# Performance work log

Hardware: AMD Instinct MI355X
Metric: run time of the kernel (lower is better)

Reference implementation:

```python
import jax, jax.numpy as jnp
import numpy as np

N_QUBITS = 6
N_LAYERS = 2
QSVT_DEGREE = 3
BATCH = 128
SEQ_LEN = 512
DIM = 2 ** N_QUBITS
# wire 0 is the most-significant bit in the statevector index (PennyLane convention)
_POP = np.array([bin(i).count('1') for i in range(DIM)], dtype=np.float32)
PHASE_SIGN = jnp.asarray(N_QUBITS - 2.0 * _POP)  # (DIM,): sum_w (1 - 2*bit_w)


def _rx(t):
    c = jnp.cos(0.5 * t).astype(jnp.complex64)
    s = (-1j * jnp.sin(0.5 * t)).astype(jnp.complex64)
    return jnp.stack([jnp.stack([c, s]), jnp.stack([s, c])])


def _ry(t):
    c = jnp.cos(0.5 * t).astype(jnp.complex64)
    s = jnp.sin(0.5 * t).astype(jnp.complex64)
    return jnp.stack([jnp.stack([c, -s]), jnp.stack([s, c])])


def _rz(t):
    e = jnp.exp(-0.5j * t.astype(jnp.complex64))
    z = jnp.zeros((), jnp.complex64)
    return jnp.stack([jnp.stack([e, z]), jnp.stack([z, jnp.conj(e)])])


def _apply_1q(psi, U, w):
    # psi: (B,) + (2,)*N_QUBITS ; U: (2,2) complex, same for all batch elems
    psi = jnp.moveaxis(psi, 1 + w, -1)
    psi = psi @ U.T
    return jnp.moveaxis(psi, -1, 1 + w)


def _apply_ry_batched(psi, theta, w):
    # RY with a per-batch angle theta: (B,)
    psi = jnp.moveaxis(psi, 1 + w, -1)
    c = jnp.cos(0.5 * theta).reshape((-1,) + (1,) * (N_QUBITS - 1))
    s = jnp.sin(0.5 * theta).reshape((-1,) + (1,) * (N_QUBITS - 1))
    a, b = psi[..., 0], psi[..., 1]
    psi = jnp.stack([c * a - s * b, s * a + c * b], axis=-1)
    return jnp.moveaxis(psi, -1, 1 + w)


def _cnot(psi, c, t):
    p0 = jax.lax.index_in_dim(psi, 0, axis=1 + c, keepdims=True)
    p1 = jax.lax.index_in_dim(psi, 1, axis=1 + c, keepdims=True)
    p1 = jnp.flip(p1, axis=1 + t)
    return jnp.concatenate([p0, p1], axis=1 + c)


def _circuit_step(h, x, params, poly):
    # h, x: (B, N_QUBITS) angles. Returns <Z_w> per qubit: (B, N_QUBITS).
    B = h.shape[0]
    # 1) state encoding: RY(h_w)|0> = cos(h/2)|0> + sin(h/2)|1>  (product state)
    c, s = jnp.cos(0.5 * h), jnp.sin(0.5 * h)
    psi = jnp.ones((B, 1), jnp.complex64)
    for w in range(N_QUBITS):
        amp = jnp.stack([c[:, w], s[:, w]], axis=-1).astype(jnp.complex64)  # (B,2)
        psi = (psi[:, :, None] * amp[:, None, :]).reshape(B, -1)
    psi = psi.reshape((B,) + (2,) * N_QUBITS)
    # 2) QSVT block: RZ(coeff*pi) on every wire fuses into one diagonal phase
    for d in range(QSVT_DEGREE + 1):
        theta = poly[d] * np.pi
        phase = jnp.exp((-0.5j) * theta * PHASE_SIGN)  # (DIM,)
        psi = (psi.reshape(B, -1) * phase[None, :]).reshape((B,) + (2,) * N_QUBITS)
        for i in range(N_QUBITS - 1):
            psi = _cnot(psi, i, i + 1)
        psi = _cnot(psi, N_QUBITS - 1, 0)  # ring closure
    # 3) variational layers: per-wire RZ@RY@RX (RX applied first), then CNOT chain
    idx = 0
    for _ in range(N_LAYERS):
        for i in range(N_QUBITS):
            U = _rz(params[idx + 2]) @ _ry(params[idx + 1]) @ _rx(params[idx])
            psi = _apply_1q(psi, U, i)
            idx += 3
        for i in range(N_QUBITS - 1):
            psi = _cnot(psi, i, i + 1)
    # 4) input injection: RY(x_w) with per-batch angles
    for w in range(N_QUBITS):
        psi = _apply_ry_batched(psi, x[:, w], w)
    # 5) measurement: <Z_w> = P(bit_w=0) - P(bit_w=1)
    p = jnp.abs(psi) ** 2
    zs = []
    for w in range(N_QUBITS):
        axes = tuple(a for a in range(1, N_QUBITS + 1) if a != 1 + w)
        pw = p.sum(axis=axes)  # (B,2)
        zs.append(pw[:, 0] - pw[:, 1])
    return jnp.stack(zs, axis=-1)


def _ssm_pass(angles, params, poly, reverse):
    a = jnp.flip(angles, axis=1) if reverse else angles
    xs = jnp.moveaxis(a, 1, 0)  # (T, B, n)
    h0 = jnp.zeros((a.shape[0], N_QUBITS), jnp.float32)

    def step(h, x):
        hn = _circuit_step(h, x, params, poly)
        return hn, hn

    _, ys = jax.lax.scan(step, h0, xs)
    out = jnp.moveaxis(ys, 0, 1)  # (B, T, n)
    return jnp.flip(out, axis=1) if reverse else out


def setup_inputs() -> dict:
    key = jax.random.key(0)
    k0, k1, k2, k3 = jax.random.split(key, 4)
    angles = jax.random.uniform(k0, (BATCH, SEQ_LEN, N_QUBITS), jnp.float32) * np.float32(np.pi)
    poly_coeffs = jax.random.normal(k1, (QSVT_DEGREE + 1,), jnp.float32) * 0.1
    fwd_params = jax.random.normal(k2, (N_QUBITS * N_LAYERS * 3,), jnp.float32) * 0.1
    bwd_params = jax.random.normal(k3, (N_QUBITS * N_LAYERS * 3,), jnp.float32) * 0.1
    fwd_coeff = jnp.full((1,), 0.5, jnp.float32)
    bwd_coeff = jnp.full((1,), 0.5, jnp.float32)
    return {'angles': angles, 'poly_coeffs': poly_coeffs, 'fwd_params': fwd_params,
            'bwd_params': bwd_params, 'fwd_coeff': fwd_coeff, 'bwd_coeff': bwd_coeff}


def reference(angles, poly_coeffs, fwd_params, bwd_params, fwd_coeff, bwd_coeff):
    h_fwd = _ssm_pass(angles, fwd_params, poly_coeffs, reverse=False)
    h_bwd = _ssm_pass(angles, bwd_params, poly_coeffs, reverse=True)
    return jax.nn.sigmoid(fwd_coeff) * h_fwd + jax.nn.sigmoid(bwd_coeff) * h_bwd
```

## Files before the change

kernel.cpp:

```cpp
#include <hip/hip_runtime.h>
#include <hip/hip_bf16.h>
#include <stdint.h>

#define BATCH 128
#define SEQ   512
#define NW    6
#define DIM   64
#define NELEM (BATCH * SEQ * NW)
#define PI_F  3.14159265358979323846f

template <int CTRL>
__device__ __forceinline__ void red_stage6(float v[6]) {
#pragma unroll
    for (int w = 0; w < 6; ++w)
        v[w] += __int_as_float(__builtin_amdgcn_update_dpp(
            0, __float_as_int(v[w]), CTRL, 0xF, 0xF, false));
}

__device__ __forceinline__ void sincos_half(float h, float& s, float& c) {
    const float u = h * h;
    c = fmaf(u, fmaf(u, fmaf(u, -2.1701389e-5f, 2.6041667e-3f), -0.125f), 1.0f);
    s = h * fmaf(u, fmaf(u, fmaf(u, -1.5501e-6f, 2.6041667e-4f), -2.0833333e-2f), 0.5f);
}

__global__ void k_detect(const uint32_t* __restrict__ a, int* __restrict__ flag) {
    __shared__ int cnt;
    if (threadIdx.x == 0) cnt = 0;
    __syncthreads();
    uint32_t w = a[threadIdx.x];
    uint32_t e = (w >> 8) & 0xFFu;
    if (e >= 0x3Au && e <= 0x41u) atomicAdd(&cnt, 1);
    __syncthreads();
    if (threadIdx.x == 0) *flag = (cnt >= 128) ? 1 : 0;
}

__device__ __forceinline__ float ldf(const void* p, int i, bool bf) {
    if (bf) {
        uint32_t u = (uint32_t)((const uint16_t*)p)[i];
        return __uint_as_float(u << 16);
    }
    return ((const float*)p)[i];
}

__global__ void k_convert(const void* ang, const void* poly, const void* fp,
                          const void* bp, const void* fc, const void* bc,
                          float* __restrict__ cs, float* __restrict__ misc,
                          const int* __restrict__ flag) {
    const bool bf = (*flag != 0);
    const int i = blockIdx.x * blockDim.x + threadIdx.x;
    if (i < NELEM) {
        float x = ldf(ang, i, bf);
        float s, c;
        __sincosf(x, &s, &c);
        cs[2 * i]     = c;
        cs[2 * i + 1] = s;
    }
    if (i < 4)                    misc[i]            = ldf(poly, i, bf);
    else if (i >= 64 && i < 100)  misc[4 + (i - 64)] = ldf(fp, i - 64, bf);
    else if (i >= 128 && i < 164) misc[40 + (i - 128)] = ldf(bp, i - 128, bf);
    else if (i == 200)            misc[76] = ldf(fc, 0, bf);
    else if (i == 201)            misc[77] = ldf(bc, 0, bf);
}

__global__ void __launch_bounds__(64) k_msetup(const float* __restrict__ misc,
                                               float* __restrict__ Mg) {
    const int p   = threadIdx.x;
    const int col = blockIdx.x & 63;
    const int dir = blockIdx.x >> 6;
    const float* poly = misc;
    const float* prm  = misc + (dir ? 40 : 4);

    float yr = (p == col) ? 1.f : 0.f;
    float yi = 0.f;

#pragma unroll
    for (int d = 0; d < 4; ++d) {
        const float th = 0.5f * PI_F * poly[d] *
                         (float)(6 - 2 * (int)__popc((unsigned)p));
        float s, c;
        __sincosf(th, &s, &c);
        const float nr = yr * c + yi * s;
        const float ni = yi * c - yr * s;
        yr = nr; yi = ni;
#pragma unroll
        for (int k = 0; k < 6; ++k) {
            const int cw = k, tw = (k + 1) % 6;
            const int src = p ^ (((p >> (5 - cw)) & 1) << (5 - tw));
            yr = __shfl(yr, src, 64);
            yi = __shfl(yi, src, 64);
        }
    }

    int idx = 0;
#pragma unroll
    for (int l = 0; l < 2; ++l) {
#pragma unroll
        for (int w = 0; w < 6; ++w) {
            float cx, sx, cy, sy, cz, sz;
            __sincosf(0.5f * prm[idx + 0], &sx, &cx);
            __sincosf(0.5f * prm[idx + 1], &sy, &cy);
            __sincosf(0.5f * prm[idx + 2], &sz, &cz);
            idx += 3;
            const float A = cy * cx, B = sy * sx, C = sy * cx, D = cy * sx;
            const float U00r = cz * A + sz * B, U00i = cz * B - sz * A;
            const float U11r = U00r,            U11i = sz * A - cz * B;
            const float Xr   = cz * C + sz * D, Xi   = sz * C - cz * D;
            const int m  = 1 << (5 - w);
            const int bb = (p >> (5 - w)) & 1;
            const float C1r = bb ? U11r : U00r;
            const float C1i = bb ? U11i : U00i;
            const float C2r = bb ? Xr : -Xr;
            const float C2i = Xi;
            const float pr = __shfl_xor(yr, m, 64);
            const float pi = __shfl_xor(yi, m, 64);
            const float nr = C1r * yr - C1i * yi + C2r * pr - C2i * pi;
            const float ni = C1r * yi + C1i * yr + C2r * pi + C2i * pr;
            yr = nr; yi = ni;
        }
#pragma unroll
        for (int k = 0; k < 5; ++k) {
            const int src = p ^ (((p >> (5 - k)) & 1) << (5 - (k + 1)));
            yr = __shfl(yr, src, 64);
            yi = __shfl(yi, src, 64);
        }
    }

    float* out = Mg + ((size_t)(dir * 64 + p) * 64 + (size_t)col) * 2;
    out[0] = yr;
    out[1] = yi;
}

__global__ void __launch_bounds__(256, 1) k_sim(const float* __restrict__ cs,
                                                const float* __restrict__ Mg,
                                                float* __restrict__ hbuf) {
    const int tid   = threadIdx.x;
    const int lane  = tid & 63;
    const int wv    = tid >> 6;
    const int chain = blockIdx.x;
    const int dir   = chain >> 7;
    const int b     = chain & 127;
    float* orow = hbuf + (size_t)dir * NELEM + (size_t)b * (SEQ * NW);
    const float* csrow = cs + (size_t)b * (SEQ * NW * 2);

    __shared__ float  cl[SEQ * 12];
    __shared__ float  zb[SEQ * 6];
    __shared__ float  xs[DIM];
    __shared__ float2 pY[4][DIM];

    {
        const float4* src = (const float4*)csrow;
        float4* dst = (float4*)cl;
#pragma unroll
        for (int k = 0; k < 6; ++k) {
            const int idx = tid + k * 256;
            dst[idx] = src[idx];
        }
    }

    float2 Mc[16];
    {
        const float2* mrow =
            (const float2*)(Mg + ((size_t)(dir * 64 + lane) * 64 + wv * 16) * 2);
#pragma unroll
        for (int k = 0; k < 16; ++k) Mc[k] = mrow[k];
    }
    __syncthreads();

    int zmask[6];
#pragma unroll
    for (int w = 0; w < 6; ++w) zmask[w] = ((lane >> (5 - w)) & 1) << 31;
    bool EB[6];
#pragma unroll
    for (int w = 0; w < 6; ++w) EB[w] = (lane >> (5 - w)) & 1;

    float h[6] = {0.f, 0.f, 0.f, 0.f, 0.f, 0.f};

    for (int t = 0; t < SEQ; ++t) {
        if (wv == 0) {
            float amp = 1.f;
#pragma unroll
            for (int w = 0; w < 6; ++w) {
                float s, c;
                sincos_half(h[w], s, c);
                amp *= EB[w] ? s : c;
            }
            xs[lane] = amp;
        }
        __syncthreads();

        {
            const float4* xc = (const float4*)(xs + wv * 16);
            const float4 x0 = xc[0], x1 = xc[1], x2 = xc[2], x3 = xc[3];
            float xv[16];
            xv[0] = x0.x; xv[1] = x0.y; xv[2]  = x0.z; xv[3]  = x0.w;
            xv[4] = x1.x; xv[5] = x1.y; xv[6]  = x1.z; xv[7]  = x1.w;
            xv[8] = x2.x; xv[9] = x2.y; xv[10] = x2.z; xv[11] = x2.w;
            xv[12] = x3.x; xv[13] = x3.y; xv[14] = x3.z; xv[15] = x3.w;
            float2 acc = {0.f, 0.f};
#pragma unroll
            for (int j = 0; j < 16; ++j) {
                acc.x = fmaf(xv[j], Mc[j].x, acc.x);
                acc.y = fmaf(xv[j], Mc[j].y, acc.y);
            }
            pY[wv][lane] = acc;
        }
        __syncthreads();

        if (wv == 0) {
            const int tin = dir ? (SEQ - 1 - t) : t;

            const float4* xr4 = (const float4*)(cl + tin * 12);
            const float4 xq0 = xr4[0], xq1 = xr4[1], xq2 = xr4[2];

            const float2 y0 = pY[0][lane], y1 = pY[1][lane];
            const float2 y2 = pY[2][lane], y3 = pY[3][lane];
            const float yr = (y0.x + y1.x) + (y2.x + y3.x);
            const float yi = (y0.y + y1.y) + (y2.y + y3.y);

            float pr[6], pi[6];
#pragma unroll
            for (int w = 0; w < 6; ++w) pr[w] = __shfl_xor(yr, 1 << (5 - w), 64);
#pragma unroll
            for (int w = 0; w < 6; ++w) pi[w] = __shfl_xor(yi, 1 << (5 - w), 64);

            const float q = yr * yr + yi * yi;
            float cxw[6], sxw[6];
            cxw[0] = xq0.x; sxw[0] = xq0.y; cxw[1] = xq0.z; sxw[1] = xq0.w;
            cxw[2] = xq1.x; sxw[2] = xq1.y; cxw[3] = xq1.z; sxw[3] = xq1.w;
            cxw[4] = xq2.x; sxw[4] = xq2.y; cxw[5] = xq2.z; sxw[5] = xq2.w;

            float v[6];
#pragma unroll
            for (int w = 0; w < 6; ++w) {
                const float ac = yr * pr[w] + yi * pi[w];
                const float sq = __int_as_float(__float_as_int(q) ^ zmask[w]);
                v[w] = cxw[w] * sq - sxw[w] * ac;
            }

            red_stage6<0x111>(v);
            red_stage6<0x112>(v);
            red_stage6<0x114>(v);
            red_stage6<0x118>(v);
            red_stage6<0x142>(v);
            red_stage6<0x143>(v);
#pragma unroll
            for (int w = 0; w < 6; ++w)
                h[w] = __int_as_float(
                    __builtin_amdgcn_readlane(__float_as_int(v[w]), 63));

            float ov = h[0];
#pragma unroll
            for (int w = 1; w < 6; ++w) ov = (lane == w) ? h[w] : ov;
            if (lane < 6) zb[tin * NW + lane] = ov;
        }
    }
    __syncthreads();

    {
        const float4* zs4 = (const float4*)zb;
        float4* go = (float4*)orow;
#pragma unroll
        for (int k = 0; k < 3; ++k) {
            const int idx = tid + k * 256;
            go[idx] = zs4[idx];
        }
    }
}

__global__ void k_combine(const float* __restrict__ hbuf,
                          const float* __restrict__ misc,
                          void* __restrict__ out, const int* __restrict__ flag) {
    const int i = blockIdx.x * blockDim.x + threadIdx.x;
    if (i >= NELEM) return;
    const float sf = 1.f / (1.f + __expf(-misc[76]));
    const float sb = 1.f / (1.f + __expf(-misc[77]));
    const float v = sf * hbuf[i] + sb * hbuf[NELEM + i];
    if (*flag) ((__hip_bfloat16*)out)[i] = __float2bfloat16(v);
    else       ((float*)out)[i] = v;
}

extern "C" void kernel_launch(void* const* d_in, const int* in_sizes, int n_in,
                              void* d_out, int out_size, void* d_ws, size_t ws_size,
                              hipStream_t stream) {
    const void* ang  = d_in[0];
    const void* poly = d_in[1];
    const void* fp   = d_in[2];
    const void* bp   = d_in[3];
    const void* fc   = d_in[4];
    const void* bc   = d_in[5];

    float* cs   = (float*)d_ws;
    float* misc = cs + 2 * NELEM;
    float* hbuf = misc + 128;
    float* Mg   = hbuf + 2 * NELEM;
    int*   flag = (int*)(Mg + 2 * 64 * 64 * 2);

    k_detect<<<1, 256, 0, stream>>>((const uint32_t*)ang, flag);
    k_convert<<<(NELEM + 255) / 256, 256, 0, stream>>>(ang, poly, fp, bp, fc, bc,
                                                       cs, misc, flag);
    k_msetup<<<128, 64, 0, stream>>>(misc, Mg);
    k_sim<<<256, 256, 0, stream>>>(cs, Mg, hbuf);
    k_combine<<<(NELEM + 255) / 256, 256, 0, stream>>>(hbuf, misc, d_out, flag);
}
```

Measured before the change: 415.9 us.

## Replicate readout across waves and double-buffer matvec partials to cut barriers

Every wave now computes the readout reduction redundantly, so each wave holds h locally and builds its own slice of the product-state amplitudes from sincos factors instead of reading a shared xs vector. The partial matvec results are double-buffered in shared memory, which cuts the per-step barriers from two to one and removes the serial wave-0-only encoding phase. The cost is redundant shuffle/DPP reduction and sincos work in all four waves, plus a little more register pressure.

Measured after the change: 374.4 us. -10.0%, faster.

```diff
diff --git a/kernel.cpp b/kernel.cpp
--- a/kernel.cpp
+++ b/kernel.cpp
@@ -144,8 +144,7 @@
 
     __shared__ float  cl[SEQ * 12];
     __shared__ float  zb[SEQ * 6];
-    __shared__ float  xs[DIM];
-    __shared__ float2 pY[4][DIM];
+    __shared__ float2 pY[2][4][DIM];
 
     {
         const float4* src = (const float4*)csrow;
@@ -164,97 +163,109 @@
 #pragma unroll
         for (int k = 0; k < 16; ++k) Mc[k] = mrow[k];
     }
+
+    int zmask[6];
+#pragma unroll
+    for (int w = 0; w < 6; ++w) zmask[w] = ((lane >> (5 - w)) & 1) << 31;
+
+    float h[6] = {0.f, 0.f, 0.f, 0.f, 0.f, 0.f};
+
+    auto encode_matvec = [&](const float hh[6], float2& acc) {
+        float cw[6], sw[6];
+#pragma unroll
+        for (int w = 0; w < 6; ++w) sincos_half(hh[w], sw[w], cw[w]);
+        const float t0 = ((wv >> 1) & 1) ? sw[0] : cw[0];
+        const float t1 = (wv & 1) ? sw[1] : cw[1];
+        const float A  = t0 * t1;
+        float gh[4], gl[4];
+        gh[0] = cw[2] * cw[3]; gh[1] = cw[2] * sw[3];
+        gh[2] = sw[2] * cw[3]; gh[3] = sw[2] * sw[3];
+        gl[0] = cw[4] * cw[5]; gl[1] = cw[4] * sw[5];
+        gl[2] = sw[4] * cw[5]; gl[3] = sw[4] * sw[5];
+#pragma unroll
+        for (int a = 0; a < 4; ++a) gh[a] *= A;
+        float2 a0 = {0.f, 0.f}, a1 = {0.f, 0.f};
+#pragma unroll
+        for (int j = 0; j < 16; ++j) {
+            const float xv = gh[j >> 2] * gl[j & 3];
+            if (j & 1) {
+                a1.x = fmaf(xv, Mc[j].x, a1.x);
+                a1.y = fmaf(xv, Mc[j].y, a1.y);
+            } else {
+                a0.x = fmaf(xv, Mc[j].x, a0.x);
+                a0.y = fmaf(xv, Mc[j].y, a0.y);
+            }
+        }
+        acc.x = a0.x + a1.x;
+        acc.y = a0.y + a1.y;
+    };
+
     __syncthreads();
 
-    int zmask[6];
-#pragma unroll
-    for (int w = 0; w < 6; ++w) zmask[w] = ((lane >> (5 - w)) & 1) << 31;
-    bool EB[6];
-#pragma unroll
-    for (int w = 0; w < 6; ++w) EB[w] = (lane >> (5 - w)) & 1;
-
-    float h[6] = {0.f, 0.f, 0.f, 0.f, 0.f, 0.f};
+    {
+        float2 acc;
+        encode_matvec(h, acc);
+        pY[0][wv][lane] = acc;
+    }
+    __syncthreads();
 
     for (int t = 0; t < SEQ; ++t) {
+        const int buf  = t & 1;
+        const int tin  = dir ? (SEQ - 1 - t) : t;
+
+        const float4* xr4 = (const float4*)(cl + tin * 12);
+        const float4 xq0 = xr4[0], xq1 = xr4[1], xq2 = xr4[2];
+
+        const float2 y0 = pY[buf][0][lane], y1 = pY[buf][1][lane];
+        const float2 y2 = pY[buf][2][lane], y3 = pY[buf][3][lane];
+        const float yr = (y0.x + y1.x) + (y2.x + y3.x);
+        const float yi = (y0.y + y1.y) + (y2.y + y3.y);
+
+        float pr[6], pi[6];
+#pragma unroll
+        for (int w = 0; w < 6; ++w) pr[w] = __shfl_xor(yr, 1 << (5 - w), 64);
+#pragma unroll
+        for (int w = 0; w < 6; ++w) pi[w] = __shfl_xor(yi, 1 << (5 - w), 64);
+
+        const float q = yr * yr + yi * yi;
+        float cxw[6], sxw[6];
+        cxw[0] = xq0.x; sxw[0] = xq0.y; cxw[1] = xq0.z; sxw[1] = xq0.w;
+        cxw[2] = xq1.x; sxw[2] = xq1.y; cxw[3] = xq1.z; sxw[3] = xq1.w;
+        cxw[4] = xq2.x; sxw[4] = xq2.y; cxw[5] = xq2.z; sxw[5] = xq2.w;
+
+        float v[6];
+#pragma unroll
+        for (int w = 0; w < 6; ++w) {
+            const float ac = yr * pr[w] + yi * pi[w];
+            const float sq = __int_as_float(__float_as_int(q) ^ zmask[w]);
+            v[w] = cxw[w] * sq - sxw[w] * ac;
+        }
+
+        red_stage6<0x111>(v);
+        red_stage6<0x112>(v);
+        red_stage6<0x114>(v);
+        red_stage6<0x118>(v);
+        red_stage6<0x142>(v);
+        red_stage6<0x143>(v);
+#pragma unroll
+        for (int w = 0; w < 6; ++w)
+            h[w] = __int_as_float(
+                __builtin_amdgcn_readlane(__float_as_int(v[w]), 63));
+
         if (wv == 0) {
-            float amp = 1.f;
-#pragma unroll
-            for (int w = 0; w < 6; ++w) {
-                float s, c;
-                sincos_half(h[w], s, c);
-                amp *= EB[w] ? s : c;
-            }
-            xs[lane] = amp;
-        }
-        __syncthreads();
-
-        {
-            const float4* xc = (const float4*)(xs + wv * 16);
-            const float4 x0 = xc[0], x1 = xc[1], x2 = xc[2], x3 = xc[3];
-            float xv[16];
-            xv[0] = x0.x; xv[1] = x0.y; xv[2]  = x0.z; xv[3]  = x0.w;
-            xv[4] = x1.x; xv[5] = x1.y; xv[6]  = x1.z; xv[7]  = x1.w;
-            xv[8] = x2.x; xv[9] = x2.y; xv[10] = x2.z; xv[11] = x2.w;
-            xv[12] = x3.x; xv[13] = x3.y; xv[14] = x3.z; xv[15] = x3.w;
-            float2 acc = {0.f, 0.f};
-#pragma unroll
-            for (int j = 0; j < 16; ++j) {
-                acc.x = fmaf(xv[j], Mc[j].x, acc.x);
-                acc.y = fmaf(xv[j], Mc[j].y, acc.y);
-            }
-            pY[wv][lane] = acc;
-        }
-        __syncthreads();
-
-        if (wv == 0) {
-            const int tin = dir ? (SEQ - 1 - t) : t;
-
-            const float4* xr4 = (const float4*)(cl + tin * 12);
-            const float4 xq0 = xr4[0], xq1 = xr4[1], xq2 = xr4[2];
-
-            const float2 y0 = pY[0][lane], y1 = pY[1][lane];
-            const float2 y2 = pY[2][lane], y3 = pY[3][lane];
-            const float yr = (y0.x + y1.x) + (y2.x + y3.x);
-            const float yi = (y0.y + y1.y) + (y2.y + y3.y);
-
-            float pr[6], pi[6];
-#pragma unroll
-            for (int w = 0; w < 6; ++w) pr[w] = __shfl_xor(yr, 1 << (5 - w), 64);
-#pragma unroll
-            for (int w = 0; w < 6; ++w) pi[w] = __shfl_xor(yi, 1 << (5 - w), 64);
-
-            const float q = yr * yr + yi * yi;
-            float cxw[6], sxw[6];
-            cxw[0] = xq0.x; sxw[0] = xq0.y; cxw[1] = xq0.z; sxw[1] = xq0.w;
-            cxw[2] = xq1.x; sxw[2] = xq1.y; cxw[3] = xq1.z; sxw[3] = xq1.w;
-            cxw[4] = xq2.x; sxw[4] = xq2.y; cxw[5] = xq2.z; sxw[5] = xq2.w;
-
-            float v[6];
-#pragma unroll
-            for (int w = 0; w < 6; ++w) {
-                const float ac = yr * pr[w] + yi * pi[w];
-                const float sq = __int_as_float(__float_as_int(q) ^ zmask[w]);
-                v[w] = cxw[w] * sq - sxw[w] * ac;
-            }
-
-            red_stage6<0x111>(v);
-            red_stage6<0x112>(v);
-            red_stage6<0x114>(v);
-            red_stage6<0x118>(v);
-            red_stage6<0x142>(v);
-            red_stage6<0x143>(v);
-#pragma unroll
-            for (int w = 0; w < 6; ++w)
-                h[w] = __int_as_float(
-                    __builtin_amdgcn_readlane(__float_as_int(v[w]), 63));
-
             float ov = h[0];
 #pragma unroll
             for (int w = 1; w < 6; ++w) ov = (lane == w) ? h[w] : ov;
             if (lane < 6) zb[tin * NW + lane] = ov;
         }
-    }
-    __syncthreads();
+
+        if (t + 1 < SEQ) {
+            float2 acc;
+            encode_matvec(h, acc);
+            pY[buf ^ 1][wv][lane] = acc;
+        }
+        __syncthreads();
+    }
 
     {
         const float4* zs4 = (const float4*)zb;
```

## Collapse per-step simulation into a single wavefront with factored product-state matvec

Applied to the files above, without the earlier changes.

The recurrent simulation kernel now runs each chain on one 64-lane wavefront instead of four waves. That removes the two block-wide barriers and the shared-memory exchanges of the product-state vector and partial sums on every time step. Each lane builds the product state as an outer product of two 8-element factors and does the full 64-column complex matvec. It reads its padded unitary row from LDS instead of holding 16 columns in registers. Per-step angle inputs are read from global memory with a one-step-ahead prefetch instead of being staged in LDS, which trades barrier latency for more per-lane ALU and LDS traffic.

Result: slower. 428.8 us (+3.1%).

```diff
diff --git a/kernel.cpp b/kernel.cpp
--- a/kernel.cpp
+++ b/kernel.cpp
@@ -8,6 +8,9 @@
 #define DIM   64
 #define NELEM (BATCH * SEQ * NW)
 #define PI_F  3.14159265358979323846f
+#define MSTRIDE 132
+
+typedef float v2f __attribute__((ext_vector_type(2)));
 
 template <int CTRL>
 __device__ __forceinline__ void red_stage6(float v[6]) {
@@ -130,129 +133,123 @@
     out[1] = yi;
 }
 
-__global__ void __launch_bounds__(256, 1) k_sim(const float* __restrict__ cs,
-                                                const float* __restrict__ Mg,
-                                                float* __restrict__ hbuf) {
-    const int tid   = threadIdx.x;
-    const int lane  = tid & 63;
-    const int wv    = tid >> 6;
+__global__ void __launch_bounds__(64, 1) k_sim(const float* __restrict__ cs,
+                                               const float* __restrict__ Mg,
+                                               float* __restrict__ hbuf) {
+    const int lane  = threadIdx.x;
     const int chain = blockIdx.x;
     const int dir   = chain >> 7;
     const int b     = chain & 127;
     float* orow = hbuf + (size_t)dir * NELEM + (size_t)b * (SEQ * NW);
     const float* csrow = cs + (size_t)b * (SEQ * NW * 2);
 
-    __shared__ float  cl[SEQ * 12];
-    __shared__ float  zb[SEQ * 6];
-    __shared__ float  xs[DIM];
-    __shared__ float2 pY[4][DIM];
+    __shared__ float Ml[DIM * MSTRIDE];
+    __shared__ float zb[SEQ * NW];
 
     {
-        const float4* src = (const float4*)csrow;
-        float4* dst = (float4*)cl;
-#pragma unroll
-        for (int k = 0; k < 6; ++k) {
-            const int idx = tid + k * 256;
-            dst[idx] = src[idx];
-        }
-    }
-
-    float2 Mc[16];
-    {
-        const float2* mrow =
-            (const float2*)(Mg + ((size_t)(dir * 64 + lane) * 64 + wv * 16) * 2);
-#pragma unroll
-        for (int k = 0; k < 16; ++k) Mc[k] = mrow[k];
+        const float4* mrow = (const float4*)(Mg + (size_t)(dir * 64 + lane) * 128);
+        float4* dst = (float4*)(Ml + lane * MSTRIDE);
+#pragma unroll
+        for (int cc = 0; cc < 32; ++cc) dst[cc] = mrow[cc];
     }
     __syncthreads();
 
     int zmask[6];
 #pragma unroll
     for (int w = 0; w < 6; ++w) zmask[w] = ((lane >> (5 - w)) & 1) << 31;
-    bool EB[6];
-#pragma unroll
-    for (int w = 0; w < 6; ++w) EB[w] = (lane >> (5 - w)) & 1;
 
     float h[6] = {0.f, 0.f, 0.f, 0.f, 0.f, 0.f};
 
+    const int tin0 = dir ? SEQ - 1 : 0;
+    const float4* x0p = (const float4*)(csrow + tin0 * 12);
+    float4 xq0 = x0p[0], xq1 = x0p[1], xq2 = x0p[2];
+
+    const float4* Mrow4 = (const float4*)(Ml + lane * MSTRIDE);
+
     for (int t = 0; t < SEQ; ++t) {
-        if (wv == 0) {
-            float amp = 1.f;
-#pragma unroll
-            for (int w = 0; w < 6; ++w) {
-                float s, c;
-                sincos_half(h[w], s, c);
-                amp *= EB[w] ? s : c;
-            }
-            xs[lane] = amp;
-        }
-        __syncthreads();
-
+        const int tin  = dir ? (SEQ - 1 - t) : t;
+        const int tn   = (t + 1 < SEQ) ? t + 1 : t;
+        const int tinn = dir ? (SEQ - 1 - tn) : tn;
+        const float4* xnp = (const float4*)(csrow + tinn * 12);
+        float4 nx0 = xnp[0], nx1 = xnp[1], nx2 = xnp[2];
+
+        float cw6[6], sw6[6];
+#pragma unroll
+        for (int w = 0; w < 6; ++w) sincos_half(h[w], sw6[w], cw6[w]);
+        float G[8], L[8];
         {
-            const float4* xc = (const float4*)(xs + wv * 16);
-            const float4 x0 = xc[0], x1 = xc[1], x2 = xc[2], x3 = xc[3];
-            float xv[16];
-            xv[0] = x0.x; xv[1] = x0.y; xv[2]  = x0.z; xv[3]  = x0.w;
-            xv[4] = x1.x; xv[5] = x1.y; xv[6]  = x1.z; xv[7]  = x1.w;
-            xv[8] = x2.x; xv[9] = x2.y; xv[10] = x2.z; xv[11] = x2.w;
-            xv[12] = x3.x; xv[13] = x3.y; xv[14] = x3.z; xv[15] = x3.w;
-            float2 acc = {0.f, 0.f};
-#pragma unroll
-            for (int j = 0; j < 16; ++j) {
-                acc.x = fmaf(xv[j], Mc[j].x, acc.x);
-                acc.y = fmaf(xv[j], Mc[j].y, acc.y);
-            }
-            pY[wv][lane] = acc;
-        }
-        __syncthreads();
-
-        if (wv == 0) {
-            const int tin = dir ? (SEQ - 1 - t) : t;
-
-            const float4* xr4 = (const float4*)(cl + tin * 12);
-            const float4 xq0 = xr4[0], xq1 = xr4[1], xq2 = xr4[2];
-
-            const float2 y0 = pY[0][lane], y1 = pY[1][lane];
-            const float2 y2 = pY[2][lane], y3 = pY[3][lane];
-            const float yr = (y0.x + y1.x) + (y2.x + y3.x);
-            const float yi = (y0.y + y1.y) + (y2.y + y3.y);
-
-            float pr[6], pi[6];
-#pragma unroll
-            for (int w = 0; w < 6; ++w) pr[w] = __shfl_xor(yr, 1 << (5 - w), 64);
-#pragma unroll
-            for (int w = 0; w < 6; ++w) pi[w] = __shfl_xor(yi, 1 << (5 - w), 64);
-
-            const float q = yr * yr + yi * yi;
-            float cxw[6], sxw[6];
-            cxw[0] = xq0.x; sxw[0] = xq0.y; cxw[1] = xq0.z; sxw[1] = xq0.w;
-            cxw[2] = xq1.x; sxw[2] = xq1.y; cxw[3] = xq1.z; sxw[3] = xq1.w;
-            cxw[4] = xq2.x; sxw[4] = xq2.y; cxw[5] = xq2.z; sxw[5] = xq2.w;
-
-            float v[6];
-#pragma unroll
-            for (int w = 0; w < 6; ++w) {
-                const float ac = yr * pr[w] + yi * pi[w];
-                const float sq = __int_as_float(__float_as_int(q) ^ zmask[w]);
-                v[w] = cxw[w] * sq - sxw[w] * ac;
-            }
-
-            red_stage6<0x111>(v);
-            red_stage6<0x112>(v);
-            red_stage6<0x114>(v);
-            red_stage6<0x118>(v);
-            red_stage6<0x142>(v);
-            red_stage6<0x143>(v);
-#pragma unroll
-            for (int w = 0; w < 6; ++w)
-                h[w] = __int_as_float(
-                    __builtin_amdgcn_readlane(__float_as_int(v[w]), 63));
-
-            float ov = h[0];
-#pragma unroll
-            for (int w = 1; w < 6; ++w) ov = (lane == w) ? h[w] : ov;
-            if (lane < 6) zb[tin * NW + lane] = ov;
-        }
+            const float g00 = cw6[0] * cw6[1], g01 = cw6[0] * sw6[1];
+            const float g10 = sw6[0] * cw6[1], g11 = sw6[0] * sw6[1];
+            G[0] = g00 * cw6[2]; G[1] = g00 * sw6[2];
+            G[2] = g01 * cw6[2]; G[3] = g01 * sw6[2];
+            G[4] = g10 * cw6[2]; G[5] = g10 * sw6[2];
+            G[6] = g11 * cw6[2]; G[7] = g11 * sw6[2];
+            const float l00 = cw6[3] * cw6[4], l01 = cw6[3] * sw6[4];
+            const float l10 = sw6[3] * cw6[4], l11 = sw6[3] * sw6[4];
+            L[0] = l00 * cw6[5]; L[1] = l00 * sw6[5];
+            L[2] = l01 * cw6[5]; L[3] = l01 * sw6[5];
+            L[4] = l10 * cw6[5]; L[5] = l10 * sw6[5];
+            L[6] = l11 * cw6[5]; L[7] = l11 * sw6[5];
+        }
+
+        v2f y = {0.f, 0.f};
+#pragma unroll
+        for (int a = 0; a < 8; ++a) {
+            const float4 c0 = Mrow4[4 * a + 0];
+            const float4 c1 = Mrow4[4 * a + 1];
+            const float4 c2 = Mrow4[4 * a + 2];
+            const float4 c3 = Mrow4[4 * a + 3];
+            v2f T = {0.f, 0.f};
+            T += L[0] * (v2f){c0.x, c0.y};
+            T += L[1] * (v2f){c0.z, c0.w};
+            T += L[2] * (v2f){c1.x, c1.y};
+            T += L[3] * (v2f){c1.z, c1.w};
+            T += L[4] * (v2f){c2.x, c2.y};
+            T += L[5] * (v2f){c2.z, c2.w};
+            T += L[6] * (v2f){c3.x, c3.y};
+            T += L[7] * (v2f){c3.z, c3.w};
+            y += G[a] * T;
+        }
+        const float yr = y.x, yi = y.y;
+
+        float pr[6], pi[6];
+#pragma unroll
+        for (int w = 0; w < 6; ++w) pr[w] = __shfl_xor(yr, 1 << (5 - w), 64);
+#pragma unroll
+        for (int w = 0; w < 6; ++w) pi[w] = __shfl_xor(yi, 1 << (5 - w), 64);
+
+        const float q = yr * yr + yi * yi;
+        float cxw[6], sxw[6];
+        cxw[0] = xq0.x; sxw[0] = xq0.y; cxw[1] = xq0.z; sxw[1] = xq0.w;
+        cxw[2] = xq1.x; sxw[2] = xq1.y; cxw[3] = xq1.z; sxw[3] = xq1.w;
+        cxw[4] = xq2.x; sxw[4] = xq2.y; cxw[5] = xq2.z; sxw[5] = xq2.w;
+
+        float v[6];
+#pragma unroll
+        for (int w = 0; w < 6; ++w) {
+            const float ac = yr * pr[w] + yi * pi[w];
+            const float sq = __int_as_float(__float_as_int(q) ^ zmask[w]);
+            v[w] = cxw[w] * sq - sxw[w] * ac;
+        }
+
+        red_stage6<0x111>(v);
+        red_stage6<0x112>(v);
+        red_stage6<0x114>(v);
+        red_stage6<0x118>(v);
+        red_stage6<0x142>(v);
+        red_stage6<0x143>(v);
+
+        if (lane == 63) {
+#pragma unroll
+            for (int w = 0; w < 6; ++w) zb[tin * NW + w] = v[w];
+        }
+
+#pragma unroll
+        for (int w = 0; w < 6; ++w)
+            h[w] = __int_as_float(
+                __builtin_amdgcn_readlane(__float_as_int(v[w]), 63));
+
+        xq0 = nx0; xq1 = nx1; xq2 = nx2;
     }
     __syncthreads();
 
@@ -260,8 +257,8 @@
         const float4* zs4 = (const float4*)zb;
         float4* go = (float4*)orow;
 #pragma unroll
-        for (int k = 0; k < 3; ++k) {
-            const int idx = tid + k * 256;
+        for (int k = 0; k < 12; ++k) {
+            const int idx = lane + k * 64;
             go[idx] = zs4[idx];
         }
     }
@@ -299,6 +296,6 @@
     k_convert<<<(NELEM + 255) / 256, 256, 0, stream>>>(ang, poly, fp, bp, fc, bc,
                                                        cs, misc, flag);
     k_msetup<<<128, 64, 0, stream>>>(misc, Mg);
-    k_sim<<<256, 256, 0, stream>>>(cs, Mg, hbuf);
+    k_sim<<<256, 64, 0, stream>>>(cs, Mg, hbuf);
     k_combine<<<(NELEM + 255) / 256, 256, 0, stream>>>(hbuf, misc, d_out, flag);
 }
```
